# Performance work log

Hardware: AMD Instinct MI355X
Metric: run time of the kernel (lower is better)

Reference implementation:

```python
import jax, jax.numpy as jnp
import numpy as np

B, N, E = 128, 2048, 32768   # events, nodes per history graph, temporal edges per graph
C, TC, H = 4, 4, 2           # channels, time_channels, heads (hardcoded in source)
DH = C // H
L = 2                        # num_layers


def setup_inputs() -> dict:
    key = jax.random.key(0)
    ks = jax.random.split(key, 16)
    return {
        "x": jax.random.normal(ks[0], (B, N, C), jnp.float32),
        "edge_index": jax.random.randint(ks[1], (B, 2, E), 0, N),
        "edge_time": jax.random.uniform(ks[2], (B, E), jnp.float32),
        "timestamp": jax.random.uniform(ks[3], (B,), jnp.float32),
        "src_index": jax.random.randint(ks[4], (B,), 0, N),
        "dst_index": jax.random.randint(ks[5], (B,), 0, N),
        "time_w": jax.random.normal(ks[6], (TC,), jnp.float32),
        "time_b": jax.random.normal(ks[7], (TC,), jnp.float32),
        "Wq": jax.random.normal(ks[8], (L, C, C), jnp.float32) / np.sqrt(C).astype(np.float32),
        "Wk": jax.random.normal(ks[9], (L, C + TC, C), jnp.float32) / np.sqrt(C + TC).astype(np.float32),
        "Wv": jax.random.normal(ks[10], (L, C + TC, C), jnp.float32) / np.sqrt(C + TC).astype(np.float32),
        "Wo": jax.random.normal(ks[11], (L, C, C), jnp.float32) / np.sqrt(C).astype(np.float32),
        "bo": jnp.zeros((L, C), jnp.float32),
        "W_lin": jax.random.normal(ks[12], (2 * C + TC, 2), jnp.float32) / np.sqrt(2 * C + TC).astype(np.float32),
        "b_lin": jnp.zeros((2,), jnp.float32),
    }


def _time_enc(t, w, b):
    # TimeEncoder: cos(t * w + b)  (Bochner-style functional time encoding)
    return jnp.cos(t[..., None] * w + b)


def _encode(x, src, dst, phi, Wq, Wk, Wv, Wo, bo):
    # seg id per edge: (batch, dst node) -> flat segment for segment softmax
    seg = (jnp.arange(B, dtype=dst.dtype)[:, None] * N + dst).reshape(-1)  # [B*E]
    h = x
    for l in range(L):
        h_src = jnp.take_along_axis(h, src[:, :, None], axis=1)            # [B,E,C] gather source feats
        msg = jnp.concatenate([h_src, phi], axis=-1)                       # [B,E,C+TC]
        q = (h @ Wq[l]).reshape(B, N, C)                                   # [B,N,C]
        k = (msg @ Wk[l]).reshape(B, E, H, DH)
        v = (msg @ Wv[l]).reshape(B, E, H, DH)
        q_e = jnp.take_along_axis(q, dst[:, :, None], axis=1).reshape(B, E, H, DH)
        logits = (q_e * k).sum(-1) / np.float32(np.sqrt(DH))               # [B,E,H]
        lf = logits.reshape(B * E, H)
        m = jax.ops.segment_max(lf, seg, num_segments=B * N)               # stable softmax max
        p = jnp.exp(lf - m[seg])
        s = jax.ops.segment_sum(p, seg, num_segments=B * N)
        agg = jax.ops.segment_sum(p[:, :, None] * v.reshape(B * E, H, DH), seg, num_segments=B * N)
        attn = (agg / jnp.where(s == 0, 1.0, s)[:, :, None]).reshape(B, N, C)
        h = jax.nn.relu(h + attn @ Wo[l] + bo[l])                          # residual + out-proj + relu
    return h


def reference(x, edge_index, edge_time, timestamp, src_index, dst_index,
              time_w, time_b, Wq, Wk, Wv, Wo, bo, W_lin, b_lin):
    src, dst = edge_index[:, 0, :], edge_index[:, 1, :]
    dt = timestamp[:, None] - edge_time                                    # [B,E] time deltas vs query time
    phi = _time_enc(dt, time_w, time_b)                                    # [B,E,TC]
    h = _encode(x, src, dst, phi, Wq, Wk, Wv, Wo, bo)                      # [B,N,C]
    bidx = jnp.arange(B)
    src_x = h[bidx, src_index]                                             # [B,C]
    dst_x = h[bidx, dst_index]                                             # [B,C]
    time_x = _time_enc(timestamp, time_w, time_b)                          # [B,TC]
    feats = jnp.concatenate([src_x, dst_x, time_x], axis=-1)               # [B,12]
    return feats @ W_lin + b_lin                                           # [B,2]
```

## Files before the change

### kernel.cpp

```cpp
#include <hip/hip_runtime.h>
#include <hip/hip_fp16.h>

namespace {

constexpr int B = 128, N = 2048, E = 32768;
constexpr int LOG2N = 11, LOG2E = 15;
constexpr int QE = 8192;
constexpr int RECCAP = 14336;
constexpr int SSTR = 16384;

constexpr size_t OFF_H0  = 0;
constexpr size_t OFF_H1  = 4u * 1024 * 1024;
constexpr size_t OFF_SRT = 8u * 1024 * 1024;
constexpr size_t OFF_SEG = 40u * 1024 * 1024;

__global__ __launch_bounds__(1024) void sort_kernel(const int* __restrict__ edge_index,
                                                    const float* __restrict__ edge_time,
                                                    const float* __restrict__ timestamp,
                                                    unsigned* __restrict__ sorted,
                                                    unsigned* __restrict__ seg) {
  __shared__ int      cnt[N];
  __shared__ int      partial[1024];
  __shared__ int      tot_s;
  __shared__ unsigned rec[RECCAP];
  int blk = blockIdx.x, b = blk >> 2, q = blk & 3, t = threadIdx.x;
  const int* src_arr = edge_index + ((size_t)(2 * b) << LOG2E) + q * QE;
  const int* dst_arr = edge_index + ((size_t)(2 * b + 1) << LOG2E) + q * QE;
  const float* et    = edge_time + ((size_t)b << LOG2E) + q * QE;
  float ts = timestamp[b];

  cnt[t] = 0; cnt[t + 1024] = 0;
  __syncthreads();

  for (int e = t; e < QE; e += 1024) atomicAdd(&cnt[dst_arr[e]], 1);
  __syncthreads();

  int i0 = 2 * t, i1 = 2 * t + 1;
  int d0 = cnt[i0], d1 = cnt[i1];
  int w0 = (d0 + 3) & ~3, w1 = (d1 + 3) & ~3;
  int sum = w0 + w1;
  partial[t] = sum;
  __syncthreads();
  for (int d = 1; d < 1024; d <<= 1) {
    int v = (t >= d) ? partial[t - d] : 0;
    __syncthreads();
    partial[t] += v;
    __syncthreads();
  }
  int run = partial[t] - sum;
  int run2 = run + w0;
  if (t == 1023) tot_s = partial[t];
  unsigned* sg = seg + (size_t)blk * N;
  sg[i0] = (unsigned)run  | ((unsigned)d0 << 16);
  sg[i1] = (unsigned)run2 | ((unsigned)d1 << 16);
  cnt[i0] = run;
  cnt[i1] = run2;
  __syncthreads();

  for (int e = t; e < QE; e += 1024) {
    int dst = dst_arr[e], src = src_arr[e];
    float dt = ts - et[e];
    unsigned hd = (unsigned)__half_as_ushort(__float2half(dt));
    int pos = atomicAdd(&cnt[dst], 1);
    rec[pos] = (unsigned)src | (hd << 16);
  }
  __syncthreads();

  int tot4 = tot_s >> 2;
  const uint4* rec4 = (const uint4*)rec;
  uint4* out4 = (uint4*)(sorted + (size_t)blk * SSTR);
  for (int i = t; i < tot4; i += 1024) out4[i] = rec4[i];
}

__global__ __launch_bounds__(256) void layer_kernel(const float4* __restrict__ h_in,
                                                    float4* __restrict__ h_out,
                                                    const unsigned* __restrict__ seg,
                                                    const unsigned* __restrict__ sorted,
                                                    const float* __restrict__ tw,
                                                    const float* __restrict__ tb,
                                                    const float* __restrict__ Wq,
                                                    const float* __restrict__ Wk,
                                                    const float* __restrict__ Wv,
                                                    const float* __restrict__ Wo,
                                                    const float* __restrict__ bo) {
  __shared__ float4 lh[N];
  int blk = blockIdx.x, b = blk >> 3, oct = blk & 7, t = threadIdx.x;

  const float4* hb = h_in + ((size_t)b << LOG2N);
#pragma unroll
  for (int j = 0; j < 8; j++) {
    int idx = j * 256 + t;
    lh[idx] = hb[idx];
  }

  float twf[4], tbf[4], bof[4], wq[16], wof[16], wk[32], wv[32];
#pragma unroll
  for (int j = 0; j < 4; j++) { twf[j] = tw[j]; tbf[j] = tb[j]; bof[j] = bo[j]; }
#pragma unroll
  for (int j = 0; j < 16; j++) { wq[j] = Wq[j]; wof[j] = Wo[j]; }
#pragma unroll
  for (int j = 0; j < 32; j++) { wk[j] = Wk[j]; wv[j] = Wv[j]; }
  __syncthreads();

  int n = (oct << 8) + t;
  float4 hn = lh[n];
  float q0 = hn.x * wq[0] + hn.y * wq[4] + hn.z * wq[8]  + hn.w * wq[12];
  float q1 = hn.x * wq[1] + hn.y * wq[5] + hn.z * wq[9]  + hn.w * wq[13];
  float q2 = hn.x * wq[2] + hn.y * wq[6] + hn.z * wq[10] + hn.w * wq[14];
  float q3 = hn.x * wq[3] + hn.y * wq[7] + hn.z * wq[11] + hn.w * wq[15];
  const float RS2 = 0.70710678118654752f;
  float u0[8], u1[8];
#pragma unroll
  for (int j = 0; j < 8; j++) {
    u0[j] = RS2 * (q0 * wk[j * 4 + 0] + q1 * wk[j * 4 + 1]);
    u1[j] = RS2 * (q2 * wk[j * 4 + 2] + q3 * wk[j * 4 + 3]);
  }

  int begq[4], degq[4];
  const uint4* sp[4];
#pragma unroll
  for (int q = 0; q < 4; ++q) {
    int qblk = (b << 2) + q;
    unsigned sd = seg[(size_t)qblk * N + n];
    begq[q] = (int)(sd & 0xFFFFu);
    degq[q] = (int)(sd >> 16);
    sp[q] = (const uint4*)(sorted + (size_t)qblk * SSTR + begq[q]);
  }
  uint4 pf[4];
#pragma unroll
  for (int q = 0; q < 4; ++q)
    pf[q] = (degq[q] > 0) ? sp[q][0] : make_uint4(0, 0, 0, 0);

  float m0 = -INFINITY, m1 = -INFINITY;
  float s0 = 0.f, s1 = 0.f, a00 = 0.f, a01 = 0.f, a10 = 0.f, a11 = 0.f;

#pragma unroll
  for (int q = 0; q < 4; ++q) {
    int dg = degq[q];
    if (dg <= 0) continue;
    int nch = (dg + 3) >> 2;
    uint4 cur = pf[q];
    for (int c = 0; c < nch; ++c) {
      uint4 nxt = (c + 1 < nch) ? sp[q][c + 1] : make_uint4(0, 0, 0, 0);
      unsigned rcs[4] = {cur.x, cur.y, cur.z, cur.w};
      int jb = c << 2;
      float l0e[4], l1e[4], v0e[4], v1e[4], v2e[4], v3e[4];
#pragma unroll
      for (int i = 0; i < 4; ++i) {
        bool valid = (jb + i) < dg;
        unsigned rcv = valid ? rcs[i] : 0u;
        int src = (int)(rcv & 0x7FFu);
        float dt = __half2float(__ushort_as_half((unsigned short)(rcv >> 16)));
        float4 hs = lh[src];
        float p0c = __cosf(dt * twf[0] + tbf[0]);
        float p1c = __cosf(dt * twf[1] + tbf[1]);
        float p2c = __cosf(dt * twf[2] + tbf[2]);
        float p3c = __cosf(dt * twf[3] + tbf[3]);
        float l0 = u0[0] * hs.x + u0[1] * hs.y + u0[2] * hs.z + u0[3] * hs.w
                 + u0[4] * p0c + u0[5] * p1c + u0[6] * p2c + u0[7] * p3c;
        float l1 = u1[0] * hs.x + u1[1] * hs.y + u1[2] * hs.z + u1[3] * hs.w
                 + u1[4] * p0c + u1[5] * p1c + u1[6] * p2c + u1[7] * p3c;
        l0e[i] = valid ? l0 : -INFINITY;
        l1e[i] = valid ? l1 : -INFINITY;
        v0e[i] = wv[0] * hs.x + wv[4] * hs.y + wv[8]  * hs.z + wv[12] * hs.w
               + wv[16] * p0c + wv[20] * p1c + wv[24] * p2c + wv[28] * p3c;
        v1e[i] = wv[1] * hs.x + wv[5] * hs.y + wv[9]  * hs.z + wv[13] * hs.w
               + wv[17] * p0c + wv[21] * p1c + wv[25] * p2c + wv[29] * p3c;
        v2e[i] = wv[2] * hs.x + wv[6] * hs.y + wv[10] * hs.z + wv[14] * hs.w
               + wv[18] * p0c + wv[22] * p1c + wv[26] * p2c + wv[30] * p3c;
        v3e[i] = wv[3] * hs.x + wv[7] * hs.y + wv[11] * hs.z + wv[15] * hs.w
               + wv[19] * p0c + wv[23] * p1c + wv[27] * p2c + wv[31] * p3c;
      }
      float lx0 = fmaxf(fmaxf(l0e[0], l0e[1]), fmaxf(l0e[2], l0e[3]));
      float nm0 = fmaxf(m0, lx0);
      float sc0 = __expf(m0 - nm0);
      float pe0 = __expf(l0e[0] - nm0), pe1 = __expf(l0e[1] - nm0);
      float pe2 = __expf(l0e[2] - nm0), pe3 = __expf(l0e[3] - nm0);
      s0  = s0  * sc0 + (pe0 + pe1 + pe2 + pe3);
      a00 = a00 * sc0 + (pe0 * v0e[0] + pe1 * v0e[1] + pe2 * v0e[2] + pe3 * v0e[3]);
      a01 = a01 * sc0 + (pe0 * v1e[0] + pe1 * v1e[1] + pe2 * v1e[2] + pe3 * v1e[3]);
      m0 = nm0;
      float lx1 = fmaxf(fmaxf(l1e[0], l1e[1]), fmaxf(l1e[2], l1e[3]));
      float nm1 = fmaxf(m1, lx1);
      float sc1 = __expf(m1 - nm1);
      float qe0 = __expf(l1e[0] - nm1), qe1 = __expf(l1e[1] - nm1);
      float qe2 = __expf(l1e[2] - nm1), qe3 = __expf(l1e[3] - nm1);
      s1  = s1  * sc1 + (qe0 + qe1 + qe2 + qe3);
      a10 = a10 * sc1 + (qe0 * v2e[0] + qe1 * v2e[1] + qe2 * v2e[2] + qe3 * v2e[3]);
      a11 = a11 * sc1 + (qe0 * v3e[0] + qe1 * v3e[1] + qe2 * v3e[2] + qe3 * v3e[3]);
      m1 = nm1;
      cur = nxt;
    }
  }
  float d0 = (s0 == 0.f) ? 1.f : s0;
  float d1 = (s1 == 0.f) ? 1.f : s1;
  float at0 = a00 / d0, at1 = a01 / d0, at2 = a10 / d1, at3 = a11 / d1;
  float o0 = bof[0] + at0 * wof[0] + at1 * wof[4] + at2 * wof[8]  + at3 * wof[12];
  float o1 = bof[1] + at0 * wof[1] + at1 * wof[5] + at2 * wof[9]  + at3 * wof[13];
  float o2 = bof[2] + at0 * wof[2] + at1 * wof[6] + at2 * wof[10] + at3 * wof[14];
  float o3 = bof[3] + at0 * wof[3] + at1 * wof[7] + at2 * wof[11] + at3 * wof[15];
  h_out[((size_t)b << LOG2N) + n] =
      make_float4(fmaxf(hn.x + o0, 0.f), fmaxf(hn.y + o1, 0.f),
                  fmaxf(hn.z + o2, 0.f), fmaxf(hn.w + o3, 0.f));
}

__global__ void final_kernel(const float4* __restrict__ h,
                             const int* __restrict__ src_index, const int* __restrict__ dst_index,
                             const float* __restrict__ timestamp,
                             const float* __restrict__ tw,
                             const float* __restrict__ tb,
                             const float* __restrict__ W_lin,
                             const float* __restrict__ b_lin,
                             float* __restrict__ out) {
  int b = threadIdx.x;
  if (b >= B) return;
  float4 sx = h[(((size_t)b) << LOG2N) + src_index[b]];
  float4 dx = h[(((size_t)b) << LOG2N) + dst_index[b]];
  float ts = timestamp[b];
  float f[12];
  f[0] = sx.x; f[1] = sx.y; f[2] = sx.z; f[3] = sx.w;
  f[4] = dx.x; f[5] = dx.y; f[6] = dx.z; f[7] = dx.w;
#pragma unroll
  for (int j = 0; j < 4; j++) f[8 + j] = __cosf(ts * tw[j] + tb[j]);
#pragma unroll
  for (int c = 0; c < 2; c++) {
    float o = b_lin[c];
#pragma unroll
    for (int j = 0; j < 12; j++) o += f[j] * W_lin[j * 2 + c];
    out[b * 2 + c] = o;
  }
}

}

extern "C" void kernel_launch(void* const* d_in, const int* in_sizes, int n_in,
                              void* d_out, int out_size, void* d_ws, size_t ws_size,
                              hipStream_t stream) {
  (void)in_sizes; (void)n_in; (void)out_size; (void)ws_size;
  const float* x         = (const float*)d_in[0];
  const int*   edge_idx  = (const int*)d_in[1];
  const float* edge_time = (const float*)d_in[2];
  const float* timestamp = (const float*)d_in[3];
  const int*   src_index = (const int*)d_in[4];
  const int*   dst_index = (const int*)d_in[5];
  const float* time_w    = (const float*)d_in[6];
  const float* time_b    = (const float*)d_in[7];
  const float* Wq        = (const float*)d_in[8];
  const float* Wk        = (const float*)d_in[9];
  const float* Wv        = (const float*)d_in[10];
  const float* Wo        = (const float*)d_in[11];
  const float* bo        = (const float*)d_in[12];
  const float* W_lin     = (const float*)d_in[13];
  const float* b_lin     = (const float*)d_in[14];

  char* ws = (char*)d_ws;
  float4*   h0     = (float4*)(ws + OFF_H0);
  float4*   h1     = (float4*)(ws + OFF_H1);
  unsigned* sorted = (unsigned*)(ws + OFF_SRT);
  unsigned* seg    = (unsigned*)(ws + OFF_SEG);

  sort_kernel<<<4 * B, 1024, 0, stream>>>(edge_idx, edge_time, timestamp, sorted, seg);

  layer_kernel<<<8 * B, 256, 0, stream>>>((const float4*)x, h1, seg, sorted,
                                          time_w, time_b,
                                          Wq + 0 * 16, Wk + 0 * 32, Wv + 0 * 32,
                                          Wo + 0 * 16, bo + 0 * 4);
  layer_kernel<<<8 * B, 256, 0, stream>>>(h1, h0, seg, sorted,
                                          time_w, time_b,
                                          Wq + 1 * 16, Wk + 1 * 32, Wv + 1 * 32,
                                          Wo + 1 * 16, bo + 1 * 4);

  final_kernel<<<1, 128, 0, stream>>>(h0, src_index, dst_index, timestamp, time_w, time_b,
                                      W_lin, b_lin, (float*)d_out);
}
```

Baseline: 202.5 us.

## Reorder nodes by in-degree to balance warps and pack FMAs into float2

Adds a rank kernel that sorts each graph's nodes by total in-degree (counting sort over 64 buckets) and writes a permuted segment table, node map and inverse map. Layer kernels then give each thread a node in degree order, so lanes in a wavefront have similar loop trip counts and less divergence. Hidden state is stored in ranked order between layers, and the final kernel maps indices back through the inverse table. The per-edge logits and values are also recast as paired float2 FMAs, which may allow packed FMA instructions. The extra kernel launch and permuted global writes add overhead.

```diff
diff --git a/kernel.cpp b/kernel.cpp
--- a/kernel.cpp
+++ b/kernel.cpp
@@ -13,6 +13,13 @@
 constexpr size_t OFF_H1  = 4u * 1024 * 1024;
 constexpr size_t OFF_SRT = 8u * 1024 * 1024;
 constexpr size_t OFF_SEG = 40u * 1024 * 1024;
+constexpr size_t OFF_SGR = 44u * 1024 * 1024;
+constexpr size_t OFF_NR  = 48u * 1024 * 1024;
+constexpr size_t OFF_INV = 49u * 1024 * 1024;
+
+__device__ __forceinline__ float2 f2fma(float a, float2 b, float2 c) {
+  return make_float2(fmaf(a, b.x, c.x), fmaf(a, b.y, c.y));
+}
 
 __global__ __launch_bounds__(1024) void sort_kernel(const int* __restrict__ edge_index,
                                                     const float* __restrict__ edge_time,
@@ -72,9 +79,53 @@
   for (int i = t; i < tot4; i += 1024) out4[i] = rec4[i];
 }
 
+__global__ __launch_bounds__(1024) void rank_kernel(const unsigned* __restrict__ seg,
+                                                    unsigned* __restrict__ segr,
+                                                    unsigned* __restrict__ nr_out,
+                                                    int* __restrict__ inv_out) {
+  __shared__ int      dhist[64];
+  __shared__ unsigned nrp[N];
+  int b = blockIdx.x, t = threadIdx.x;
+  if (t < 64) dhist[t] = 0;
+  __syncthreads();
+  int n0 = t, n1 = t + 1024;
+  int deg0 = 0, deg1 = 0;
+#pragma unroll
+  for (int q = 0; q < 4; q++) {
+    deg0 += (int)(seg[(size_t)((b << 2) + q) * N + n0] >> 16);
+    deg1 += (int)(seg[(size_t)((b << 2) + q) * N + n1] >> 16);
+  }
+  atomicAdd(&dhist[min(deg0, 63)], 1);
+  atomicAdd(&dhist[min(deg1, 63)], 1);
+  __syncthreads();
+  if (t == 0) {
+    int acc = 0;
+    for (int k = 0; k < 64; k++) { int c = dhist[k]; dhist[k] = acc; acc += c; }
+  }
+  __syncthreads();
+  int r0 = atomicAdd(&dhist[min(deg0, 63)], 1);
+  int r1 = atomicAdd(&dhist[min(deg1, 63)], 1);
+  nrp[r0] = (unsigned)n0;
+  nrp[r1] = (unsigned)n1;
+  inv_out[((size_t)b << LOG2N) + n0] = r0;
+  inv_out[((size_t)b << LOG2N) + n1] = r1;
+  __syncthreads();
+#pragma unroll
+  for (int i = 0; i < 2; i++) {
+    int r = t + (i << 10);
+    unsigned node = nrp[r];
+    nr_out[((size_t)b << LOG2N) + r] = node;
+#pragma unroll
+    for (int q = 0; q < 4; q++)
+      segr[(size_t)((b << 2) + q) * N + r] = seg[(size_t)((b << 2) + q) * N + node];
+  }
+}
+
 __global__ __launch_bounds__(256) void layer_kernel(const float4* __restrict__ h_in,
+                                                    int in_ranked,
                                                     float4* __restrict__ h_out,
-                                                    const unsigned* __restrict__ seg,
+                                                    const unsigned* __restrict__ nr_g,
+                                                    const unsigned* __restrict__ segr,
                                                     const unsigned* __restrict__ sorted,
                                                     const float* __restrict__ tw,
                                                     const float* __restrict__ tb,
@@ -86,42 +137,49 @@
   __shared__ float4 lh[N];
   int blk = blockIdx.x, b = blk >> 3, oct = blk & 7, t = threadIdx.x;
 
-  const float4* hb = h_in + ((size_t)b << LOG2N);
+  const float4*   hb = h_in + ((size_t)b << LOG2N);
+  const unsigned* nb = nr_g + ((size_t)b << LOG2N);
 #pragma unroll
   for (int j = 0; j < 8; j++) {
     int idx = j * 256 + t;
-    lh[idx] = hb[idx];
-  }
-
-  float twf[4], tbf[4], bof[4], wq[16], wof[16], wk[32], wv[32];
+    int node = in_ranked ? (int)nb[idx] : idx;
+    lh[node] = hb[idx];
+  }
+  int n = (int)nb[(oct << 8) + t];
+
+  float twf[4], tbf[4], bof[4], wq[16], wof[16], wk[32];
+  float2 wv01[8], wv23[8];
 #pragma unroll
   for (int j = 0; j < 4; j++) { twf[j] = tw[j]; tbf[j] = tb[j]; bof[j] = bo[j]; }
 #pragma unroll
   for (int j = 0; j < 16; j++) { wq[j] = Wq[j]; wof[j] = Wo[j]; }
 #pragma unroll
-  for (int j = 0; j < 32; j++) { wk[j] = Wk[j]; wv[j] = Wv[j]; }
-  __syncthreads();
-
-  int n = (oct << 8) + t;
+  for (int j = 0; j < 32; j++) wk[j] = Wk[j];
+#pragma unroll
+  for (int j = 0; j < 8; j++) {
+    wv01[j] = make_float2(Wv[j * 4 + 0], Wv[j * 4 + 1]);
+    wv23[j] = make_float2(Wv[j * 4 + 2], Wv[j * 4 + 3]);
+  }
+  __syncthreads();
+
   float4 hn = lh[n];
   float q0 = hn.x * wq[0] + hn.y * wq[4] + hn.z * wq[8]  + hn.w * wq[12];
   float q1 = hn.x * wq[1] + hn.y * wq[5] + hn.z * wq[9]  + hn.w * wq[13];
   float q2 = hn.x * wq[2] + hn.y * wq[6] + hn.z * wq[10] + hn.w * wq[14];
   float q3 = hn.x * wq[3] + hn.y * wq[7] + hn.z * wq[11] + hn.w * wq[15];
   const float RS2 = 0.70710678118654752f;
-  float u0[8], u1[8];
-#pragma unroll
-  for (int j = 0; j < 8; j++) {
-    u0[j] = RS2 * (q0 * wk[j * 4 + 0] + q1 * wk[j * 4 + 1]);
-    u1[j] = RS2 * (q2 * wk[j * 4 + 2] + q3 * wk[j * 4 + 3]);
-  }
+  float2 u01[8];
+#pragma unroll
+  for (int j = 0; j < 8; j++)
+    u01[j] = make_float2(RS2 * (q0 * wk[j * 4 + 0] + q1 * wk[j * 4 + 1]),
+                         RS2 * (q2 * wk[j * 4 + 2] + q3 * wk[j * 4 + 3]));
 
   int begq[4], degq[4];
   const uint4* sp[4];
 #pragma unroll
   for (int q = 0; q < 4; ++q) {
     int qblk = (b << 2) + q;
-    unsigned sd = seg[(size_t)qblk * N + n];
+    unsigned sd = segr[(size_t)qblk * N + (oct << 8) + t];
     begq[q] = (int)(sd & 0xFFFFu);
     degq[q] = (int)(sd >> 16);
     sp[q] = (const uint4*)(sorted + (size_t)qblk * SSTR + begq[q]);
@@ -156,20 +214,19 @@
         float p1c = __cosf(dt * twf[1] + tbf[1]);
         float p2c = __cosf(dt * twf[2] + tbf[2]);
         float p3c = __cosf(dt * twf[3] + tbf[3]);
-        float l0 = u0[0] * hs.x + u0[1] * hs.y + u0[2] * hs.z + u0[3] * hs.w
-                 + u0[4] * p0c + u0[5] * p1c + u0[6] * p2c + u0[7] * p3c;
-        float l1 = u1[0] * hs.x + u1[1] * hs.y + u1[2] * hs.z + u1[3] * hs.w
-                 + u1[4] * p0c + u1[5] * p1c + u1[6] * p2c + u1[7] * p3c;
-        l0e[i] = valid ? l0 : -INFINITY;
-        l1e[i] = valid ? l1 : -INFINITY;
-        v0e[i] = wv[0] * hs.x + wv[4] * hs.y + wv[8]  * hs.z + wv[12] * hs.w
-               + wv[16] * p0c + wv[20] * p1c + wv[24] * p2c + wv[28] * p3c;
-        v1e[i] = wv[1] * hs.x + wv[5] * hs.y + wv[9]  * hs.z + wv[13] * hs.w
-               + wv[17] * p0c + wv[21] * p1c + wv[25] * p2c + wv[29] * p3c;
-        v2e[i] = wv[2] * hs.x + wv[6] * hs.y + wv[10] * hs.z + wv[14] * hs.w
-               + wv[18] * p0c + wv[22] * p1c + wv[26] * p2c + wv[30] * p3c;
-        v3e[i] = wv[3] * hs.x + wv[7] * hs.y + wv[11] * hs.z + wv[15] * hs.w
-               + wv[19] * p0c + wv[23] * p1c + wv[27] * p2c + wv[31] * p3c;
+        float2 l01 = make_float2(0.f, 0.f), v01 = make_float2(0.f, 0.f),
+               v23 = make_float2(0.f, 0.f);
+        l01 = f2fma(hs.x, u01[0], l01); v01 = f2fma(hs.x, wv01[0], v01); v23 = f2fma(hs.x, wv23[0], v23);
+        l01 = f2fma(hs.y, u01[1], l01); v01 = f2fma(hs.y, wv01[1], v01); v23 = f2fma(hs.y, wv23[1], v23);
+        l01 = f2fma(hs.z, u01[2], l01); v01 = f2fma(hs.z, wv01[2], v01); v23 = f2fma(hs.z, wv23[2], v23);
+        l01 = f2fma(hs.w, u01[3], l01); v01 = f2fma(hs.w, wv01[3], v01); v23 = f2fma(hs.w, wv23[3], v23);
+        l01 = f2fma(p0c,  u01[4], l01); v01 = f2fma(p0c,  wv01[4], v01); v23 = f2fma(p0c,  wv23[4], v23);
+        l01 = f2fma(p1c,  u01[5], l01); v01 = f2fma(p1c,  wv01[5], v01); v23 = f2fma(p1c,  wv23[5], v23);
+        l01 = f2fma(p2c,  u01[6], l01); v01 = f2fma(p2c,  wv01[6], v01); v23 = f2fma(p2c,  wv23[6], v23);
+        l01 = f2fma(p3c,  u01[7], l01); v01 = f2fma(p3c,  wv01[7], v01); v23 = f2fma(p3c,  wv23[7], v23);
+        l0e[i] = valid ? l01.x : -INFINITY;
+        l1e[i] = valid ? l01.y : -INFINITY;
+        v0e[i] = v01.x; v1e[i] = v01.y; v2e[i] = v23.x; v3e[i] = v23.y;
       }
       float lx0 = fmaxf(fmaxf(l0e[0], l0e[1]), fmaxf(l0e[2], l0e[3]));
       float nm0 = fmaxf(m0, lx0);
@@ -199,12 +256,13 @@
   float o1 = bof[1] + at0 * wof[1] + at1 * wof[5] + at2 * wof[9]  + at3 * wof[13];
   float o2 = bof[2] + at0 * wof[2] + at1 * wof[6] + at2 * wof[10] + at3 * wof[14];
   float o3 = bof[3] + at0 * wof[3] + at1 * wof[7] + at2 * wof[11] + at3 * wof[15];
-  h_out[((size_t)b << LOG2N) + n] =
+  h_out[((size_t)b << LOG2N) + (oct << 8) + t] =
       make_float4(fmaxf(hn.x + o0, 0.f), fmaxf(hn.y + o1, 0.f),
                   fmaxf(hn.z + o2, 0.f), fmaxf(hn.w + o3, 0.f));
 }
 
 __global__ void final_kernel(const float4* __restrict__ h,
+                             const int* __restrict__ inv,
                              const int* __restrict__ src_index, const int* __restrict__ dst_index,
                              const float* __restrict__ timestamp,
                              const float* __restrict__ tw,
@@ -214,8 +272,10 @@
                              float* __restrict__ out) {
   int b = threadIdx.x;
   if (b >= B) return;
-  float4 sx = h[(((size_t)b) << LOG2N) + src_index[b]];
-  float4 dx = h[(((size_t)b) << LOG2N) + dst_index[b]];
+  int rs = inv[((size_t)b << LOG2N) + src_index[b]];
+  int rd = inv[((size_t)b << LOG2N) + dst_index[b]];
+  float4 sx = h[((size_t)b << LOG2N) + rs];
+  float4 dx = h[((size_t)b << LOG2N) + rd];
   float ts = timestamp[b];
   float f[12];
   f[0] = sx.x; f[1] = sx.y; f[2] = sx.z; f[3] = sx.w;
@@ -258,18 +318,22 @@
   float4*   h1     = (float4*)(ws + OFF_H1);
   unsigned* sorted = (unsigned*)(ws + OFF_SRT);
   unsigned* seg    = (unsigned*)(ws + OFF_SEG);
+  unsigned* segr   = (unsigned*)(ws + OFF_SGR);
+  unsigned* nr     = (unsigned*)(ws + OFF_NR);
+  int*      inv    = (int*)(ws + OFF_INV);
 
   sort_kernel<<<4 * B, 1024, 0, stream>>>(edge_idx, edge_time, timestamp, sorted, seg);
-
-  layer_kernel<<<8 * B, 256, 0, stream>>>((const float4*)x, h1, seg, sorted,
+  rank_kernel<<<B, 1024, 0, stream>>>(seg, segr, nr, inv);
+
+  layer_kernel<<<8 * B, 256, 0, stream>>>((const float4*)x, 0, h1, nr, segr, sorted,
                                           time_w, time_b,
                                           Wq + 0 * 16, Wk + 0 * 32, Wv + 0 * 32,
                                           Wo + 0 * 16, bo + 0 * 4);
-  layer_kernel<<<8 * B, 256, 0, stream>>>(h1, h0, seg, sorted,
+  layer_kernel<<<8 * B, 256, 0, stream>>>(h1, 1, h0, nr, segr, sorted,
                                           time_w, time_b,
                                           Wq + 1 * 16, Wk + 1 * 32, Wv + 1 * 32,
                                           Wo + 1 * 16, bo + 1 * 4);
 
-  final_kernel<<<1, 128, 0, stream>>>(h0, src_index, dst_index, timestamp, time_w, time_b,
-                                      W_lin, b_lin, (float*)d_out);
-}
+  final_kernel<<<1, 128, 0, stream>>>(h0, inv, src_index, dst_index, timestamp,
+                                      time_w, time_b, W_lin, b_lin, (float*)d_out);
+}
```

Measured after the change: 222.9 us. 10.1% more time.
